# Kernel tuning notes

Measured on AMD Instinct MI355X. Metric: run time of the kernel, lower is better.

## Reference

```python
import jax, jax.numpy as jnp
import numpy as np

H = 1024           # hidden_dim
BS = 32            # batch size
STEPS = 128        # number of chart steps
AMB = 32           # ambiguous decompositions per cell (padded fixed)
START = 256        # start_index: number of pre-filled leaf entries
CHART_LEN = START + STEPS


def setup_inputs() -> dict:
    key = jax.random.key(0)
    k1, k2, k3, k4 = jax.random.split(key, 4)
    chart = jax.random.normal(k1, (BS, CHART_LEN, 2 * H), dtype=jnp.float32)
    # (l, r) child positions per step/batch/ambiguity; valid filled entries in [0, START)
    operations = jax.random.randint(k2, (STEPS, BS, AMB, 2), 0, START, dtype=jnp.int32)
    U = jax.random.uniform(k3, (5 * H, 2 * H), dtype=jnp.float32)
    b = jnp.zeros((5 * H,), dtype=jnp.float32)
    energy_u = jax.random.uniform(k4, (H,), dtype=jnp.float32)
    return {"chart": chart, "operations": operations, "start_index": START,
            "U": U, "b": b, "energy_u": energy_u}


def reference(chart, operations, start_index, U, b, energy_u):
    h_dim = energy_u.shape[0]
    bs, amb = chart.shape[0], operations.shape[2]
    batch_idx = jnp.arange(bs)[:, None, None]  # [bs,1,1] for gather broadcast
    temperature = jnp.float32(1.0)
    eps = jnp.float32(1e-8)  # torch cosine_similarity eps
    u_norm = jnp.maximum(jnp.linalg.norm(energy_u), eps)

    def step_fn(ch, inp):
        step, ops = inp  # ops: [bs, amb, 2]
        # gather child chart entries: [bs, amb, 2, 2H]
        entries = ch[batch_idx, ops, :]
        ccL = entries[:, :, 0, :h_dim]                 # left cell state  [bs,amb,H]
        ccR = entries[:, :, 1, :h_dim]                 # right cell state [bs,amb,H]
        hh = entries[:, :, :, h_dim:].reshape(bs, amb, 2 * h_dim)  # [hL;hR]
        preact = jnp.einsum('bah,gh->bag', hh, U) + b  # [bs,amb,5H]
        i  = jax.nn.sigmoid(preact[..., :h_dim])
        fL = jax.nn.sigmoid(preact[..., h_dim:2 * h_dim])
        fR = jax.nn.sigmoid(preact[..., 2 * h_dim:3 * h_dim])
        o  = jax.nn.sigmoid(preact[..., 3 * h_dim:4 * h_dim])
        u  = jnp.tanh(preact[..., 4 * h_dim:])
        c = fL * ccL + fR * ccR + i * u                # [bs,amb,H]
        h = o * jnp.tanh(c)                            # [bs,amb,H]
        # cosine-similarity energy against learned vector energy_u
        h_norm = jnp.maximum(jnp.linalg.norm(h, axis=2), eps)  # [bs,amb]
        e = (h @ energy_u) / (u_norm * h_norm)                 # [bs,amb]
        s = jax.nn.softmax(e / temperature, axis=1)[..., None] # [bs,amb,1]
        combined = jnp.concatenate([(s * c).sum(axis=1), (s * h).sum(axis=1)], axis=-1)
        ch = ch.at[:, start_index + step, :].set(combined)
        return ch, None

    n_steps = operations.shape[0]
    chart, _ = jax.lax.scan(step_fn, chart, (jnp.arange(n_steps), operations))
    return chart
```

## Files before the change

### kernel.cpp

```cpp
#include <hip/hip_runtime.h>
#include <hip/hip_fp16.h>


typedef unsigned int u32;
typedef unsigned short u16;
typedef __attribute__((ext_vector_type(8))) short short8;
typedef __attribute__((ext_vector_type(4))) float f32x4;
typedef __attribute__((ext_vector_type(4))) u16 u16x4;
typedef _Float16 h8 __attribute__((ext_vector_type(8)));
typedef _Float16 h2v __attribute__((ext_vector_type(2)));
typedef _Float16 h4v __attribute__((ext_vector_type(4)));

#define CHART_ROWS 384
#define L2E 1.4426950408889634f

__device__ __forceinline__ u16 f2bf(float f) {
  u32 u = __float_as_uint(f);
  u32 r = u + 0x7fffu + ((u >> 16) & 1u);
  return (u16)(r >> 16);
}

__device__ __forceinline__ h2v pk_exp2(h2v x) {
  __half2 t = *(__half2*)&x;
  t = h2exp2(t);
  return *(h2v*)&t;
}
__device__ __forceinline__ h2v pk_rcp(h2v x) {
  __half2 t = *(__half2*)&x;
  t = h2rcp(t);
  return *(h2v*)&t;
}

#if __has_builtin(__builtin_amdgcn_fdot2)
__device__ __forceinline__ float fdot2a(h2v a, h2v b, float c) {
  return __builtin_amdgcn_fdot2(a, b, c, false);
}
#else
__device__ __forceinline__ float fdot2a(h2v a, h2v b, float c) {
  return c + (float)a[0] * (float)b[0] + (float)a[1] * (float)b[1];
}
#endif

__device__ __forceinline__ void async16(const void* g, void* l) {
  __builtin_amdgcn_global_load_lds((const __attribute__((address_space(1))) u32*)g,
                                   (__attribute__((address_space(3))) u32*)l, 16, 0, 0);
}

#define BAR() __builtin_amdgcn_s_barrier()
#define VMCNT4 asm volatile("s_waitcnt vmcnt(4)" ::: "memory")
#define VMCNT0 asm volatile("s_waitcnt vmcnt(0)" ::: "memory")

__global__ void k_cvt_u(const float4* __restrict__ U4, u16* __restrict__ Ubf) {
  int i = blockIdx.x * blockDim.x + threadIdx.x;
  int row = i >> 9;
  float sc = (row < 4096) ? -L2E : (2.0f * L2E);
  float4 v = U4[i];
  u16x4 o = {f2bf(v.x * sc), f2bf(v.y * sc), f2bf(v.z * sc), f2bf(v.w * sc)};
  *(u16x4*)(Ubf + (size_t)i * 4) = o;
}

__global__ void k_cvt_chart(const float* __restrict__ chart,
                            u16* __restrict__ chb, _Float16* __restrict__ chc,
                            float* __restrict__ out) {
  int i = blockIdx.x * blockDim.x + threadIdx.x;
  int row = i >> 8;
  int k4 = (i & 255) * 4;
  int b = row >> 8, op = row & 255;
  const size_t base = (size_t)(b * CHART_ROWS + op) * 2048;
  const float4 vh = *(const float4*)(chart + base + 1024 + k4);
  const float4 vc = *(const float4*)(chart + base + k4);
  u16x4 oh = {f2bf(vh.x), f2bf(vh.y), f2bf(vh.z), f2bf(vh.w)};
  h4v oc = {(_Float16)vc.x, (_Float16)vc.y, (_Float16)vc.z, (_Float16)vc.w};
  *(u16x4*)(chb + (size_t)row * 1024 + k4) = oh;
  *(h4v*)(chc + (size_t)row * 1024 + k4) = oc;
  *(float4*)(out + base + k4) = vc;
  *(float4*)(out + base + 1024 + k4) = vh;
}

#define LOAD_A(BUFO, MH) do { \
  _Pragma("unroll") \
  for (int i_ = 0; i_ < 4; ++i_) { \
    a[0][i_] = *(const short8*)(As + (BUFO) + am + (MH)*4096 + i_*1024 + sl0); \
    a[1][i_] = *(const short8*)(As + (BUFO) + am + (MH)*4096 + i_*1024 + sl1); \
  } } while (0)

#define LOAD_B(BUFO, NH, BR) do { \
  _Pragma("unroll") \
  for (int j_ = 0; j_ < 2; ++j_) { \
    BR[0][j_] = *(const short8*)(Bs + (BUFO) + bm + (NH)*2048 + j_*1024 + sl0); \
    BR[1][j_] = *(const short8*)(Bs + (BUFO) + bm + (NH)*2048 + j_*1024 + sl1); \
  } } while (0)

#define MFMA_Q(MH, NH, BR) do { \
  __builtin_amdgcn_s_setprio(1); \
  _Pragma("unroll") \
  for (int kk_ = 0; kk_ < 2; ++kk_) \
    _Pragma("unroll") \
    for (int i_ = 0; i_ < 4; ++i_) \
      _Pragma("unroll") \
      for (int j_ = 0; j_ < 2; ++j_) \
        acc[(MH)*4+i_][(NH)*2+j_] = __builtin_amdgcn_mfma_f32_16x16x32_bf16( \
            a[kk_][i_], BR[kk_][j_], acc[(MH)*4+i_][(NH)*2+j_], 0, 0, 0); \
  __builtin_amdgcn_s_setprio(0); } while (0)

__global__ __launch_bounds__(512, 2) void k_gemm_p(
    const u16* __restrict__ chb, const u16* __restrict__ Ubf,
    const float* __restrict__ bias, _Float16* __restrict__ P, int bgh_base)
{
  __shared__ u16 As[2 * 256 * 64];
  __shared__ u16 Bs[2 * 256 * 64];

  const int tid = threadIdx.x;
  const int wid = tid >> 6, lane = tid & 63;
  const int lane15 = lane & 15, quad = lane >> 4;
  const int wr = wid >> 2, wc = wid & 3;

  const int nwg = gridDim.x * gridDim.y;
  const int flat = blockIdx.y * gridDim.x + blockIdx.x;
  const int swz = (flat & 7) * (nwg >> 3) + (flat >> 3);
  const int bx = swz % 20;
  const int by = swz / 20;
  const int bghl = by >> 3;
  const int bgh = bgh_base + bghl;
  const int bg = bgh >> 1, uhalf = bgh & 1;
  const int mtile = by & 7;

  const u16* aSrc[2]; const u16* bSrc[2]; int dOff[2];
#pragma unroll
  for (int rnd = 0; rnd < 2; ++rnd) {
    int idx = rnd * 512 + tid;
    int r = idx >> 3, s = idx & 7, c = s ^ (r & 7);
    aSrc[rnd] = chb + (size_t)(bg * 2048 + mtile * 256 + r) * 1024 + c * 8;
    bSrc[rnd] = Ubf + (size_t)(bx * 256 + r) * 2048 + uhalf * 1024 + c * 8;
    dOff[rnd] = idx * 8;
  }
  auto STAGE_A = [&](int buf, int h, int T) {
#pragma unroll
    for (int rnd = 0; rnd < 2; ++rnd)
      async16(aSrc[rnd] + (size_t)h * 131072 + T * 64,
              As + buf * 16384 + h * 8192 + dOff[rnd]);
  };
  auto STAGE_B = [&](int buf, int h, int T) {
#pragma unroll
    for (int rnd = 0; rnd < 2; ++rnd)
      async16(bSrc[rnd] + (size_t)h * 262144 + T * 64,
              Bs + buf * 16384 + h * 8192 + dOff[rnd]);
  };

  const int sl0 = ((0 * 4 + quad) ^ (lane15 & 7)) * 8;
  const int sl1 = ((1 * 4 + quad) ^ (lane15 & 7)) * 8;
  const int am = (wr * 128 + lane15) * 64;
  const int bm = (wc * 64 + lane15) * 64;

  f32x4 acc[8][4];
#pragma unroll
  for (int m_ = 0; m_ < 8; ++m_)
#pragma unroll
    for (int n_ = 0; n_ < 4; ++n_) acc[m_][n_] = (f32x4){0.f, 0.f, 0.f, 0.f};

  short8 a[2][4], b0[2][2], b1[2][2];

  STAGE_B(0, 0, 0); STAGE_B(0, 1, 0); STAGE_A(0, 0, 0); STAGE_A(0, 1, 0);
  STAGE_B(1, 0, 1); STAGE_B(1, 1, 1);
  VMCNT4;
  BAR();

  for (int it = 0; it < 8; ++it) {
    const int T1 = 2 * it + 1, T2 = 2 * it + 2, T3 = 2 * it + 3;
    const bool e2 = (T2 < 16), e3 = (T3 < 16);
    LOAD_A(0, 0); LOAD_B(0, 0, b0);
    STAGE_A(1, 0, T1);
    BAR(); MFMA_Q(0, 0, b0); BAR();

    LOAD_B(0, 1, b1);
    STAGE_A(1, 1, T1);
    BAR(); MFMA_Q(0, 1, b1); BAR();

    LOAD_A(0, 1);
    if (e2) STAGE_B(0, 0, T2);
    BAR(); MFMA_Q(1, 0, b0); BAR();

    if (e2) STAGE_B(0, 1, T2);
    BAR(); MFMA_Q(1, 1, b1);
    if (e2) { VMCNT4; } else { VMCNT0; }
    BAR();
    LOAD_A(16384, 0); LOAD_B(16384, 0, b0);
    if (e2) STAGE_A(0, 0, T2);
    BAR(); MFMA_Q(0, 0, b0); BAR();

    LOAD_B(16384, 1, b1);
    if (e2) STAGE_A(0, 1, T2);
    BAR(); MFMA_Q(0, 1, b1); BAR();

    LOAD_A(16384, 1);
    if (e3) STAGE_B(1, 0, T3);
    BAR(); MFMA_Q(1, 0, b0); BAR();

    if (e3) STAGE_B(1, 1, T3);
    BAR(); MFMA_Q(1, 1, b1);
    if (e3) { VMCNT4; }
    BAR();
  }

  float bb[4];
#pragma unroll
  for (int nt = 0; nt < 4; ++nt) {
    int g = bx * 256 + wc * 64 + nt * 16 + lane15;
    float sc = (g < 4096) ? -L2E : (2.0f * L2E);
    bb[nt] = (uhalf == 0) ? bias[g] * sc : 0.f;
  }
  _Float16* Pb = P + ((size_t)bghl * 2048 + mtile * 256 + wr * 128) * 5120
               + bx * 256 + wc * 64;
#pragma unroll
  for (int mt = 0; mt < 8; ++mt)
#pragma unroll
    for (int rg = 0; rg < 4; ++rg) {
      _Float16* pr = Pb + (size_t)(mt * 16 + quad * 4 + rg) * 5120;
#pragma unroll
      for (int nt = 0; nt < 4; ++nt)
        pr[nt * 16 + lane15] = (_Float16)(acc[mt][nt][rg] + bb[nt]);
    }
}

__global__ __launch_bounds__(256, 2) void k_fused(
    const _Float16* __restrict__ chc, const _Float16* __restrict__ P,
    const int* __restrict__ ops, const float* __restrict__ eu,
    float* __restrict__ out, int bg0)
{
  __shared__ float rS[4 * 2048];
  __shared__ float sS[4];

  const int tid = threadIdx.x;
  const int wave = tid >> 6, lane = tid & 63;
  const int flat = blockIdx.x;
  const int b_local = flat & 7;
  const int idx = flat >> 3;
  const int step = idx & 127;
  const int bgl = idx >> 7;
  const int b = (bg0 + bgl) * 8 + b_local;
  const size_t HSLAB = (size_t)2048 * 5120;
  const _Float16* Pl = P + (size_t)(2 * bgl) * HSLAB;

  float uf[2][8];
#pragma unroll
  for (int sub = 0; sub < 2; ++sub) {
    *(float4*)&uf[sub][0] = *(const float4*)(eu + sub * 512 + lane * 8);
    *(float4*)&uf[sub][4] = *(const float4*)(eu + sub * 512 + lane * 8 + 4);
  }
  float part = 0.f;
#pragma unroll
  for (int sub = 0; sub < 2; ++sub)
#pragma unroll
    for (int j = 0; j < 8; ++j) part += uf[sub][j] * uf[sub][j];
#pragma unroll
  for (int m = 1; m < 64; m <<= 1) part += __shfl_xor(part, m, 64);
  const float unorm = fmaxf(sqrtf(part), 1e-8f);
  h2v uu2[2][4];
#pragma unroll
  for (int sub = 0; sub < 2; ++sub)
#pragma unroll
    for (int p = 0; p < 4; ++p)
      uu2[sub][p] = (h2v){(_Float16)uf[sub][2 * p], (_Float16)uf[sub][2 * p + 1]};

  const h2v one2 = {(_Float16)1.0f, (_Float16)1.0f};
  const h2v m2h  = {(_Float16)(-2.0f), (_Float16)(-2.0f)};
  const h2v k2c  = {(_Float16)(2.0f * L2E), (_Float16)(2.0f * L2E)};

  float Sc[2][8], Sh[2][8];
#pragma unroll
  for (int sub = 0; sub < 2; ++sub)
#pragma unroll
    for (int j = 0; j < 8; ++j) { Sc[sub][j] = 0.f; Sh[sub][j] = 0.f; }
  float Ssum = 0.f;

  for (int rr = 0; rr < 8; ++rr) {
    const int a = wave * 8 + rr;
    const long opflat = (((long)step * 32 + b) * 32 + a) * 2;
    const int opL = ops[opflat], opR = ops[opflat + 1];
    const _Float16* PLp = Pl + (size_t)(b_local * 256 + opL) * 5120;
    const _Float16* PRp = Pl + HSLAB + (size_t)(b_local * 256 + opR) * 5120;
    const _Float16* ccL = chc + (size_t)(b * 256 + opL) * 1024;
    const _Float16* ccR = chc + (size_t)(b * 256 + opR) * 1024;
    float dot = 0.f, nn = 0.f;
    h2v cv[2][4], hv[2][4];
#pragma unroll
    for (int sub = 0; sub < 2; ++sub) {
      const int cb = sub * 512 + lane * 8;
      h2v pr2[5][4];
#pragma unroll
      for (int q = 0; q < 5; ++q) {
        h8 t8 = *(const h8*)(PLp + q * 1024 + cb) + *(const h8*)(PRp + q * 1024 + cb);
        *(h8*)&pr2[q][0] = t8;
      }
      h2v cl2[4], cr2[4];
      *(h8*)&cl2[0] = *(const h8*)(ccL + cb);
      *(h8*)&cr2[0] = *(const h8*)(ccR + cb);
#pragma unroll
      for (int p = 0; p < 4; ++p) {
        h2v sI = pk_rcp(one2 + pk_exp2(pr2[0][p]));
        h2v sL = pk_rcp(one2 + pk_exp2(pr2[1][p]));
        h2v sR = pk_rcp(one2 + pk_exp2(pr2[2][p]));
        h2v sO = pk_rcp(one2 + pk_exp2(pr2[3][p]));
        h2v rU = pk_rcp(one2 + pk_exp2(pr2[4][p]));
        h2v tU = one2 + m2h * rU;
        h2v c2 = sL * cl2[p] + sR * cr2[p] + sI * tU;
        h2v rC = pk_rcp(one2 + pk_exp2(c2 * k2c));
        h2v tC = one2 + m2h * rC;
        h2v hx = sO * tC;
        cv[sub][p] = c2; hv[sub][p] = hx;
        dot = fdot2a(hx, uu2[sub][p], dot);
        nn  = fdot2a(hx, hx, nn);
      }
    }
#pragma unroll
    for (int m = 1; m < 64; m <<= 1) {
      dot += __shfl_xor(dot, m, 64);
      nn  += __shfl_xor(nn, m, 64);
    }
    const float e = dot / (unorm * fmaxf(sqrtf(nn), 1e-8f));
    const float w = __builtin_amdgcn_exp2f(e * L2E);
    Ssum += w;
#pragma unroll
    for (int sub = 0; sub < 2; ++sub)
#pragma unroll
      for (int p = 0; p < 4; ++p) {
        Sc[sub][2 * p]     += w * (float)cv[sub][p][0];
        Sc[sub][2 * p + 1] += w * (float)cv[sub][p][1];
        Sh[sub][2 * p]     += w * (float)hv[sub][p][0];
        Sh[sub][2 * p + 1] += w * (float)hv[sub][p][1];
      }
  }

  if (lane == 0) sS[wave] = Ssum;
#pragma unroll
  for (int sub = 0; sub < 2; ++sub) {
    const int cb = sub * 512 + lane * 8;
    *(float4*)&rS[wave * 2048 + cb]            = *(float4*)&Sc[sub][0];
    *(float4*)&rS[wave * 2048 + cb + 4]        = *(float4*)&Sc[sub][4];
    *(float4*)&rS[wave * 2048 + 1024 + cb]     = *(float4*)&Sh[sub][0];
    *(float4*)&rS[wave * 2048 + 1024 + cb + 4] = *(float4*)&Sh[sub][4];
  }
  __syncthreads();

  const float inv = 1.0f / (sS[0] + sS[1] + sS[2] + sS[3]);
  float* orow = out + ((size_t)b * CHART_ROWS + 256 + step) * 2048;
#pragma unroll
  for (int half = 0; half < 2; ++half) {
#pragma unroll
    for (int sub = 0; sub < 2; ++sub) {
      const int cb = sub * 512 + lane * 8;
      const int off = half * 1024 + cb;
      float s0 = 0.f, s1 = 0.f, s2 = 0.f, s3 = 0.f;
      float s4 = 0.f, s5 = 0.f, s6 = 0.f, s7 = 0.f;
#pragma unroll
      for (int w8 = 0; w8 < 4; ++w8) {
        const float4 v0 = *(const float4*)&rS[w8 * 2048 + off];
        const float4 v1 = *(const float4*)&rS[w8 * 2048 + off + 4];
        s0 += v0.x; s1 += v0.y; s2 += v0.z; s3 += v0.w;
        s4 += v1.x; s5 += v1.y; s6 += v1.z; s7 += v1.w;
      }
      *(float4*)(orow + off)     = make_float4(s0 * inv, s1 * inv, s2 * inv, s3 * inv);
      *(float4*)(orow + off + 4) = make_float4(s4 * inv, s5 * inv, s6 * inv, s7 * inv);
    }
  }
}

extern "C" void kernel_launch(void* const* d_in, const int* in_sizes, int n_in,
                              void* d_out, int out_size, void* d_ws, size_t ws_size,
                              hipStream_t stream) {
  (void)in_sizes; (void)n_in; (void)out_size;
  const float* chart = (const float*)d_in[0];
  const int*   ops   = (const int*)d_in[1];
  const float* U     = (const float*)d_in[3];
  const float* bias  = (const float*)d_in[4];
  const float* eu    = (const float*)d_in[5];
  float* out = (float*)d_out;
  char* ws = (char*)d_ws;

  u16*      Ubf = (u16*)ws;
  u16*      chb = (u16*)(ws + 20971520);
  _Float16* chc = (_Float16*)(ws + 37748736);
  _Float16* P   = (_Float16*)(ws + 54525952);
  const size_t SLAB = (size_t)2048 * 5120;
  const bool big = ws_size >= (size_t)54525952 + 8 * SLAB * 2;

  k_cvt_u<<<10240, 256, 0, stream>>>((const float4*)U, Ubf);
  k_cvt_chart<<<8192, 256, 0, stream>>>(chart, chb, chc, out);

  if (big) {
    k_gemm_p<<<dim3(20, 64), 512, 0, stream>>>(chb, Ubf, bias, P, 0);
    k_fused<<<4096, 256, 0, stream>>>(chc, P, ops, eu, out, 0);
  } else {
    for (int bg = 0; bg < 4; ++bg) {
      k_gemm_p<<<dim3(20, 16), 512, 0, stream>>>(chb, Ubf, bias, P, 2 * bg);
      k_fused<<<1024, 256, 0, stream>>>(chc, P, ops, eu, out, bg);
    }
  }
}
```

Measured before the change: 592.2 us.

## Double fused-kernel block to 512 threads with fewer rows per wave

Grows the fused gather/gate kernel from 4 to 8 waves per block, so each wave handles 4 ambiguity rows instead of 8. All ops indices are preloaded up front, and both column halves of every row are processed in separate passes so more independent loads are in flight. The cross-wave reduction now goes through shared memory in two rounds (c, then h) with extra barriers, keeping the LDS footprint unchanged. This trades higher register pressure and more synchronisation for more memory-level parallelism on the random row gathers.

```diff
diff --git a/kernel.cpp b/kernel.cpp
--- a/kernel.cpp
+++ b/kernel.cpp
@@ -222,13 +222,13 @@
     }
 }
 
-__global__ __launch_bounds__(256, 2) void k_fused(
+__global__ __launch_bounds__(512, 2) void k_fused(
     const _Float16* __restrict__ chc, const _Float16* __restrict__ P,
     const int* __restrict__ ops, const float* __restrict__ eu,
     float* __restrict__ out, int bg0)
 {
-  __shared__ float rS[4 * 2048];
-  __shared__ float sS[4];
+  __shared__ float rS[8 * 1024];
+  __shared__ float sS[8];
 
   const int tid = threadIdx.x;
   const int wave = tid >> 6, lane = tid & 63;
@@ -266,6 +266,14 @@
   const h2v m2h  = {(_Float16)(-2.0f), (_Float16)(-2.0f)};
   const h2v k2c  = {(_Float16)(2.0f * L2E), (_Float16)(2.0f * L2E)};
 
+  int opLr[4], opRr[4];
+#pragma unroll
+  for (int rr = 0; rr < 4; ++rr) {
+    const int a = wave * 4 + rr;
+    const long opflat = (((long)step * 32 + b) * 32 + a) * 2;
+    opLr[rr] = ops[opflat]; opRr[rr] = ops[opflat + 1];
+  }
+
   float Sc[2][8], Sh[2][8];
 #pragma unroll
   for (int sub = 0; sub < 2; ++sub)
@@ -273,44 +281,74 @@
     for (int j = 0; j < 8; ++j) { Sc[sub][j] = 0.f; Sh[sub][j] = 0.f; }
   float Ssum = 0.f;
 
-  for (int rr = 0; rr < 8; ++rr) {
-    const int a = wave * 8 + rr;
-    const long opflat = (((long)step * 32 + b) * 32 + a) * 2;
-    const int opL = ops[opflat], opR = ops[opflat + 1];
-    const _Float16* PLp = Pl + (size_t)(b_local * 256 + opL) * 5120;
-    const _Float16* PRp = Pl + HSLAB + (size_t)(b_local * 256 + opR) * 5120;
-    const _Float16* ccL = chc + (size_t)(b * 256 + opL) * 1024;
-    const _Float16* ccR = chc + (size_t)(b * 256 + opR) * 1024;
+  h2v pc0[4][4], ph0[4][4];
+  float dotP[4], nnP[4];
+
+#pragma unroll
+  for (int rr = 0; rr < 4; ++rr) {
+    const int cb = 0 * 512 + lane * 8;
+    const _Float16* PLp = Pl + (size_t)(b_local * 256 + opLr[rr]) * 5120 + cb;
+    const _Float16* PRp = Pl + HSLAB + (size_t)(b_local * 256 + opRr[rr]) * 5120 + cb;
+    h2v pr2[5][4];
+#pragma unroll
+    for (int q = 0; q < 5; ++q) {
+      h8 t8 = *(const h8*)(PLp + q * 1024) + *(const h8*)(PRp + q * 1024);
+      *(h8*)&pr2[q][0] = t8;
+    }
+    h2v cl2[4], cr2[4];
+    *(h8*)&cl2[0] = *(const h8*)(chc + (size_t)(b * 256 + opLr[rr]) * 1024 + cb);
+    *(h8*)&cr2[0] = *(const h8*)(chc + (size_t)(b * 256 + opRr[rr]) * 1024 + cb);
     float dot = 0.f, nn = 0.f;
-    h2v cv[2][4], hv[2][4];
-#pragma unroll
-    for (int sub = 0; sub < 2; ++sub) {
-      const int cb = sub * 512 + lane * 8;
-      h2v pr2[5][4];
-#pragma unroll
-      for (int q = 0; q < 5; ++q) {
-        h8 t8 = *(const h8*)(PLp + q * 1024 + cb) + *(const h8*)(PRp + q * 1024 + cb);
-        *(h8*)&pr2[q][0] = t8;
-      }
-      h2v cl2[4], cr2[4];
-      *(h8*)&cl2[0] = *(const h8*)(ccL + cb);
-      *(h8*)&cr2[0] = *(const h8*)(ccR + cb);
-#pragma unroll
-      for (int p = 0; p < 4; ++p) {
-        h2v sI = pk_rcp(one2 + pk_exp2(pr2[0][p]));
-        h2v sL = pk_rcp(one2 + pk_exp2(pr2[1][p]));
-        h2v sR = pk_rcp(one2 + pk_exp2(pr2[2][p]));
-        h2v sO = pk_rcp(one2 + pk_exp2(pr2[3][p]));
-        h2v rU = pk_rcp(one2 + pk_exp2(pr2[4][p]));
-        h2v tU = one2 + m2h * rU;
-        h2v c2 = sL * cl2[p] + sR * cr2[p] + sI * tU;
-        h2v rC = pk_rcp(one2 + pk_exp2(c2 * k2c));
-        h2v tC = one2 + m2h * rC;
-        h2v hx = sO * tC;
-        cv[sub][p] = c2; hv[sub][p] = hx;
-        dot = fdot2a(hx, uu2[sub][p], dot);
-        nn  = fdot2a(hx, hx, nn);
-      }
+#pragma unroll
+    for (int p = 0; p < 4; ++p) {
+      h2v sI = pk_rcp(one2 + pk_exp2(pr2[0][p]));
+      h2v sL = pk_rcp(one2 + pk_exp2(pr2[1][p]));
+      h2v sR = pk_rcp(one2 + pk_exp2(pr2[2][p]));
+      h2v sO = pk_rcp(one2 + pk_exp2(pr2[3][p]));
+      h2v rU = pk_rcp(one2 + pk_exp2(pr2[4][p]));
+      h2v tU = one2 + m2h * rU;
+      h2v c2 = sL * cl2[p] + sR * cr2[p] + sI * tU;
+      h2v rC = pk_rcp(one2 + pk_exp2(c2 * k2c));
+      h2v tC = one2 + m2h * rC;
+      h2v hx = sO * tC;
+      pc0[rr][p] = c2; ph0[rr][p] = hx;
+      dot = fdot2a(hx, uu2[0][p], dot);
+      nn  = fdot2a(hx, hx, nn);
+    }
+    dotP[rr] = dot; nnP[rr] = nn;
+  }
+
+#pragma unroll
+  for (int rr = 0; rr < 4; ++rr) {
+    const int cb = 1 * 512 + lane * 8;
+    const _Float16* PLp = Pl + (size_t)(b_local * 256 + opLr[rr]) * 5120 + cb;
+    const _Float16* PRp = Pl + HSLAB + (size_t)(b_local * 256 + opRr[rr]) * 5120 + cb;
+    h2v pr2[5][4];
+#pragma unroll
+    for (int q = 0; q < 5; ++q) {
+      h8 t8 = *(const h8*)(PLp + q * 1024) + *(const h8*)(PRp + q * 1024);
+      *(h8*)&pr2[q][0] = t8;
+    }
+    h2v cl2[4], cr2[4];
+    *(h8*)&cl2[0] = *(const h8*)(chc + (size_t)(b * 256 + opLr[rr]) * 1024 + cb);
+    *(h8*)&cr2[0] = *(const h8*)(chc + (size_t)(b * 256 + opRr[rr]) * 1024 + cb);
+    float dot = dotP[rr], nn = nnP[rr];
+    h2v cv1[4], hv1[4];
+#pragma unroll
+    for (int p = 0; p < 4; ++p) {
+      h2v sI = pk_rcp(one2 + pk_exp2(pr2[0][p]));
+      h2v sL = pk_rcp(one2 + pk_exp2(pr2[1][p]));
+      h2v sR = pk_rcp(one2 + pk_exp2(pr2[2][p]));
+      h2v sO = pk_rcp(one2 + pk_exp2(pr2[3][p]));
+      h2v rU = pk_rcp(one2 + pk_exp2(pr2[4][p]));
+      h2v tU = one2 + m2h * rU;
+      h2v c2 = sL * cl2[p] + sR * cr2[p] + sI * tU;
+      h2v rC = pk_rcp(one2 + pk_exp2(c2 * k2c));
+      h2v tC = one2 + m2h * rC;
+      h2v hx = sO * tC;
+      cv1[p] = c2; hv1[p] = hx;
+      dot = fdot2a(hx, uu2[1][p], dot);
+      nn  = fdot2a(hx, hx, nn);
     }
 #pragma unroll
     for (int m = 1; m < 64; m <<= 1) {
@@ -321,47 +359,63 @@
     const float w = __builtin_amdgcn_exp2f(e * L2E);
     Ssum += w;
 #pragma unroll
-    for (int sub = 0; sub < 2; ++sub)
-#pragma unroll
-      for (int p = 0; p < 4; ++p) {
-        Sc[sub][2 * p]     += w * (float)cv[sub][p][0];
-        Sc[sub][2 * p + 1] += w * (float)cv[sub][p][1];
-        Sh[sub][2 * p]     += w * (float)hv[sub][p][0];
-        Sh[sub][2 * p + 1] += w * (float)hv[sub][p][1];
-      }
+    for (int p = 0; p < 4; ++p) {
+      Sc[0][2 * p]     += w * (float)pc0[rr][p][0];
+      Sc[0][2 * p + 1] += w * (float)pc0[rr][p][1];
+      Sh[0][2 * p]     += w * (float)ph0[rr][p][0];
+      Sh[0][2 * p + 1] += w * (float)ph0[rr][p][1];
+      Sc[1][2 * p]     += w * (float)cv1[p][0];
+      Sc[1][2 * p + 1] += w * (float)cv1[p][1];
+      Sh[1][2 * p]     += w * (float)hv1[p][0];
+      Sh[1][2 * p + 1] += w * (float)hv1[p][1];
+    }
   }
 
   if (lane == 0) sS[wave] = Ssum;
+  float* orow = out + ((size_t)b * CHART_ROWS + 256 + step) * 2048;
+
 #pragma unroll
   for (int sub = 0; sub < 2; ++sub) {
     const int cb = sub * 512 + lane * 8;
-    *(float4*)&rS[wave * 2048 + cb]            = *(float4*)&Sc[sub][0];
-    *(float4*)&rS[wave * 2048 + cb + 4]        = *(float4*)&Sc[sub][4];
-    *(float4*)&rS[wave * 2048 + 1024 + cb]     = *(float4*)&Sh[sub][0];
-    *(float4*)&rS[wave * 2048 + 1024 + cb + 4] = *(float4*)&Sh[sub][4];
+    *(float4*)&rS[wave * 1024 + cb]     = *(float4*)&Sc[sub][0];
+    *(float4*)&rS[wave * 1024 + cb + 4] = *(float4*)&Sc[sub][4];
   }
   __syncthreads();
-
-  const float inv = 1.0f / (sS[0] + sS[1] + sS[2] + sS[3]);
-  float* orow = out + ((size_t)b * CHART_ROWS + 256 + step) * 2048;
-#pragma unroll
-  for (int half = 0; half < 2; ++half) {
-#pragma unroll
-    for (int sub = 0; sub < 2; ++sub) {
-      const int cb = sub * 512 + lane * 8;
-      const int off = half * 1024 + cb;
-      float s0 = 0.f, s1 = 0.f, s2 = 0.f, s3 = 0.f;
-      float s4 = 0.f, s5 = 0.f, s6 = 0.f, s7 = 0.f;
-#pragma unroll
-      for (int w8 = 0; w8 < 4; ++w8) {
-        const float4 v0 = *(const float4*)&rS[w8 * 2048 + off];
-        const float4 v1 = *(const float4*)&rS[w8 * 2048 + off + 4];
-        s0 += v0.x; s1 += v0.y; s2 += v0.z; s3 += v0.w;
-        s4 += v1.x; s5 += v1.y; s6 += v1.z; s7 += v1.w;
-      }
-      *(float4*)(orow + off)     = make_float4(s0 * inv, s1 * inv, s2 * inv, s3 * inv);
-      *(float4*)(orow + off + 4) = make_float4(s4 * inv, s5 * inv, s6 * inv, s7 * inv);
-    }
+  float inv;
+  {
+    float s = 0.f;
+#pragma unroll
+    for (int w8 = 0; w8 < 8; ++w8) s += sS[w8];
+    inv = 1.0f / s;
+  }
+  {
+    const int g0 = tid * 2;
+    float s0 = 0.f, s1 = 0.f;
+#pragma unroll
+    for (int w8 = 0; w8 < 8; ++w8) {
+      const float2 v = *(const float2*)&rS[w8 * 1024 + g0];
+      s0 += v.x; s1 += v.y;
+    }
+    *(float2*)(orow + g0) = make_float2(s0 * inv, s1 * inv);
+  }
+  __syncthreads();
+
+#pragma unroll
+  for (int sub = 0; sub < 2; ++sub) {
+    const int cb = sub * 512 + lane * 8;
+    *(float4*)&rS[wave * 1024 + cb]     = *(float4*)&Sh[sub][0];
+    *(float4*)&rS[wave * 1024 + cb + 4] = *(float4*)&Sh[sub][4];
+  }
+  __syncthreads();
+  {
+    const int g0 = tid * 2;
+    float s0 = 0.f, s1 = 0.f;
+#pragma unroll
+    for (int w8 = 0; w8 < 8; ++w8) {
+      const float2 v = *(const float2*)&rS[w8 * 1024 + g0];
+      s0 += v.x; s1 += v.y;
+    }
+    *(float2*)(orow + 1024 + g0) = make_float2(s0 * inv, s1 * inv);
   }
 }
 
@@ -389,11 +443,11 @@
 
   if (big) {
     k_gemm_p<<<dim3(20, 64), 512, 0, stream>>>(chb, Ubf, bias, P, 0);
-    k_fused<<<4096, 256, 0, stream>>>(chc, P, ops, eu, out, 0);
+    k_fused<<<4096, 512, 0, stream>>>(chc, P, ops, eu, out, 0);
   } else {
     for (int bg = 0; bg < 4; ++bg) {
       k_gemm_p<<<dim3(20, 16), 512, 0, stream>>>(chb, Ubf, bias, P, 2 * bg);
-      k_fused<<<1024, 256, 0, stream>>>(chc, P, ops, eu, out, bg);
-    }
-  }
-}
+      k_fused<<<1024, 512, 0, stream>>>(chc, P, ops, eu, out, bg);
+    }
+  }
+}
```

After: 609.8 us. +3.0%, slower.
